# Kernel optimization log

Measured on AMD Instinct MI355X. Metric: run time of the kernel, lower is better.

Reference implementation:

```python
import jax, jax.numpy as jnp
import numpy as np

B, T, D, H = 2, 2048, 1024, 16
HD = D // H  # head dim = 64

def setup_inputs() -> dict:
    key = jax.random.key(0)
    k1, k2, k3 = jax.random.split(key, 3)
    x = jax.random.normal(k1, (B, T, D), dtype=jnp.float32)
    W_qkv = jax.random.normal(k2, (D, 3 * D), dtype=jnp.float32) * 0.02
    b_qkv = jax.random.normal(k3, (3 * D,), dtype=jnp.float32) * 0.02
    return {"x": x, "W_qkv": W_qkv, "b_qkv": b_qkv}

def reference(x, W_qkv, b_qkv):
    Bc, Tc, C = x.shape
    qkv = x @ W_qkv + b_qkv                     # [B,T,3D]
    q, k, v = jnp.split(qkv, 3, axis=-1)        # each [B,T,D]
    def to_heads(t):
        return t.reshape(Bc, Tc, H, HD).transpose(0, 2, 1, 3)  # [B,H,T,hd]
    q, k, v = to_heads(q), to_heads(k), to_heads(v)
    scale = 1.0 / jnp.sqrt(jnp.asarray(HD, dtype=x.dtype))
    att = jnp.einsum('bhqd,bhkd->bhqk', q, k) * scale  # [B,H,T,T]
    att = jax.nn.softmax(att, axis=-1)
    y = jnp.einsum('bhqk,bhkd->bhqd', att, v)          # [B,H,T,hd]
    return y.transpose(0, 2, 1, 3).reshape(Bc, Tc, C)
```

## Files before the change

### kernel.cpp

```cpp
#include <hip/hip_runtime.h>
#include <cstdint>

typedef unsigned short u16;
typedef __bf16 bf16x8 __attribute__((ext_vector_type(8)));
typedef float f32x4 __attribute__((ext_vector_type(4)));
typedef u16 u16x4 __attribute__((ext_vector_type(4)));
typedef u16 u16x8 __attribute__((ext_vector_type(8)));

static __device__ __forceinline__ u16 f2bf(float f) {
  return __builtin_bit_cast(u16, (__bf16)f);
}
static __device__ __forceinline__ float fexp2(float x) {
  float r;
  asm("v_exp_f32 %0, %1" : "=v"(r) : "v"(x));
  return r;
}

#define GLOAD16(gsrc, ldst) \
  __builtin_amdgcn_global_load_lds((const __attribute__((address_space(1))) void*)(gsrc), \
                                   (__attribute__((address_space(3))) void*)(ldst), 16, 0, 0)

#define WAIT_BAR_VM(n) do { \
    __builtin_amdgcn_sched_barrier(0); \
    asm volatile("s_waitcnt vmcnt(" #n ")" ::: "memory"); \
    __builtin_amdgcn_s_barrier(); \
    __builtin_amdgcn_sched_barrier(0); \
  } while (0)
#define WAIT_BAR_LGKM() do { \
    __builtin_amdgcn_sched_barrier(0); \
    asm volatile("s_waitcnt lgkmcnt(0)" ::: "memory"); \
    __builtin_amdgcn_s_barrier(); \
    __builtin_amdgcn_sched_barrier(0); \
  } while (0)

#define WV_VM(n) do { \
    __builtin_amdgcn_sched_barrier(0); \
    asm volatile("s_waitcnt vmcnt(" #n ")" ::: "memory"); \
    __builtin_amdgcn_sched_barrier(0); \
  } while (0)
#define WV_LGKM() do { \
    __builtin_amdgcn_sched_barrier(0); \
    asm volatile("s_waitcnt lgkmcnt(0)" ::: "memory"); \
    __builtin_amdgcn_sched_barrier(0); \
  } while (0)


__global__ __launch_bounds__(256) void k_prep(const float* __restrict__ x,
                                              const float* __restrict__ W,
                                              u16* __restrict__ xbf,
                                              u16* __restrict__ Wt) {
  __shared__ __align__(16) u16 tile[64 * 72];
  int t = threadIdx.x;
  if (blockIdx.x < 2048) {
    int idx = blockIdx.x * 256 + t;
    const float4* xv = (const float4*)x;
    float4 a = xv[(size_t)idx * 2];
    float4 b = xv[(size_t)idx * 2 + 1];
    u16x8 o;
    o[0]=f2bf(a.x); o[1]=f2bf(a.y); o[2]=f2bf(a.z); o[3]=f2bf(a.w);
    o[4]=f2bf(b.x); o[5]=f2bf(b.y); o[6]=f2bf(b.z); o[7]=f2bf(b.w);
    *(u16x8*)(xbf + (size_t)idx * 8) = o;
    return;
  }
  int bid = blockIdx.x - 2048;
  int bk = bid & 15, bn = bid >> 4;
  int k0 = bk * 64, n0 = bn * 64;
  #pragma unroll
  for (int r = 0; r < 4; r++) {
    int id = r * 256 + t;
    int kl = id >> 4;
    int c  = (id & 15) * 4;
    float4 v = *(const float4*)(W + (size_t)(k0 + kl) * 3072 + n0 + c);
    u16x4 o; o[0]=f2bf(v.x); o[1]=f2bf(v.y); o[2]=f2bf(v.z); o[3]=f2bf(v.w);
    *(u16x4*)(tile + kl * 72 + c) = o;
  }
  __syncthreads();
  #pragma unroll
  for (int r = 0; r < 2; r++) {
    int id = r * 256 + t;
    int nl = id >> 3;
    int w  = id & 7;
    u16x8 o;
    #pragma unroll
    for (int i = 0; i < 8; i++) o[i] = tile[(w * 8 + i) * 72 + nl];
    *(u16x8*)(Wt + (size_t)(n0 + nl) * 1024 + k0 + w * 8) = o;
  }
}

__global__ __launch_bounds__(256, 2) void k_gemm_qkv(const u16* __restrict__ xbf,
                                                     const u16* __restrict__ wt,
                                                     const float* __restrict__ bias,
                                                     u16* __restrict__ qkv,
                                                     u16* __restrict__ vT) {
  __shared__ __align__(16) u16 As[2 * 128 * 64];
  __shared__ __align__(16) u16 Bs[2 * 192 * 64];
  int wg = blockIdx.x;
  int swz = (wg & 7) * 64 + (wg >> 3);
  int mt = swz >> 4, nt = swz & 15;
  int m0 = mt * 128, n0 = nt * 192;
  int t = threadIdx.x;
  int lane = t & 63, wid = t >> 6;
  int wm = wid >> 1, wn = wid & 1;
  int g = lane >> 4, li = lane & 15;

  f32x4 acc[4][6];
  #pragma unroll
  for (int i = 0; i < 4; i++)
    #pragma unroll
    for (int j = 0; j < 6; j++) acc[i][j] = (f32x4){0.f, 0.f, 0.f, 0.f};

  auto stage = [&](int kt, int buf) {
    char* ad = (char*)As + buf * 16384;
    char* bd = (char*)Bs + buf * 24576;
    #pragma unroll
    for (int i = 0; i < 4; i++) {
      int p = t + i * 256;
      int row = p >> 3, ug = (p & 7) ^ (row & 7);
      GLOAD16(xbf + (size_t)(m0 + row) * 1024 + kt * 64 + ug * 8, ad + p * 16);
    }
    #pragma unroll
    for (int i = 0; i < 6; i++) {
      int p = t + i * 256;
      int row = p >> 3, ug = (p & 7) ^ (row & 7);
      GLOAD16(wt + (size_t)(n0 + row) * 1024 + kt * 64 + ug * 8, bd + p * 16);
    }
  };

  stage(0, 0);
  for (int kt = 0; kt < 16; ++kt) {
    if (kt < 15) {
      stage(kt + 1, (kt & 1) ^ 1);
      WAIT_BAR_VM(10);
    } else {
      WAIT_BAR_VM(0);
    }
    const char* ab = (const char*)As + (kt & 1) * 16384;
    const char* bb = (const char*)Bs + (kt & 1) * 24576;

    #pragma unroll
    for (int kk = 0; kk < 2; ++kk) {
      bf16x8 af[4], bfr[6];
      #pragma unroll
      for (int mi = 0; mi < 4; mi++) {
        int row = wm * 64 + mi * 16 + li;
        int u = (kk * 4 + g) ^ (row & 7);
        af[mi] = *(const bf16x8*)(ab + row * 128 + u * 16);
      }
      #pragma unroll
      for (int ni = 0; ni < 6; ni++) {
        int row = wn * 96 + ni * 16 + li;
        int u = (kk * 4 + g) ^ (row & 7);
        bfr[ni] = *(const bf16x8*)(bb + row * 128 + u * 16);
      }
      __builtin_amdgcn_s_setprio(1);
      #pragma unroll
      for (int mi = 0; mi < 4; mi++)
        #pragma unroll
        for (int ni = 0; ni < 6; ni++)
          acc[mi][ni] = __builtin_amdgcn_mfma_f32_16x16x32_bf16(af[mi], bfr[ni], acc[mi][ni], 0, 0, 0);
      __builtin_amdgcn_s_setprio(0);
    }

    WAIT_BAR_LGKM();
  }

  int b = m0 >> 11;
  int tbase = m0 & 2047;
  #pragma unroll
  for (int ni = 0; ni < 6; ni++) {
    int col = n0 + wn * 96 + ni * 16 + li;
    float bv = bias[col];
    float sc = (col < 1024) ? 0.18033688011112042f : 1.0f;
    #pragma unroll
    for (int mi = 0; mi < 4; mi++) {
      int trow = tbase + wm * 64 + mi * 16 + g * 4;
      if (col < 2048) {
        #pragma unroll
        for (int j = 0; j < 4; j++) {
          float v = (acc[mi][ni][j] + bv) * sc;
          qkv[(size_t)(b * 2048 + trow + j) * 3072 + col] = f2bf(v);
        }
      } else {
        u16x4 o;
        #pragma unroll
        for (int j = 0; j < 4; j++) o[j] = f2bf(acc[mi][ni][j] + bv);
        *(u16x4*)(vT + ((size_t)(b * 1024 + (col - 2048))) * 2048 + trow) = o;
      }
    }
  }
}

__global__ __launch_bounds__(128, 2) void k_attn(const u16* __restrict__ qkv,
                                                 const u16* __restrict__ vT,
                                                 float* __restrict__ out) {
  __shared__ __align__(16) u16 smem[16384];
  int bid = blockIdx.x;
  int bh = bid & 31, qt = bid >> 5;
  int b = bh >> 4, h = bh & 15;
  int qbase = qt * 64;
  int t = threadIdx.x, lane = t & 63, wave = t >> 6;
  int g = lane >> 4, li = lane & 15;

  bf16x8 q[4][2];
  #pragma unroll
  for (int qf = 0; qf < 4; qf++) {
    size_t qrow = (size_t)(b * 2048 + qbase + qf * 16 + li) * 3072 + h * 64;
    q[qf][0] = *(const bf16x8*)(qkv + qrow + g * 8);
    q[qf][1] = *(const bf16x8*)(qkv + qrow + 32 + g * 8);
  }

  f32x4 o[4][4];
  #pragma unroll
  for (int i = 0; i < 4; i++)
    #pragma unroll
    for (int j = 0; j < 4; j++) o[i][j] = (f32x4){0.f, 0.f, 0.f, 0.f};
  float la[4] = {0.f, 0.f, 0.f, 0.f};

  const u16* kbase_g = qkv + (size_t)(b * 2048 + wave * 1024) * 3072 + 1024 + h * 64;
  const u16* vbase_g = vT + (size_t)(bh * 64) * 2048 + wave * 1024;

  int r0 = lane >> 3, uu = lane & 7;
  int kuo = (uu ^ (r0 & 7)) * 8;
  int kR[8];
  #pragma unroll
  for (int i = 0; i < 8; i++) {
    int r = r0 + 8 * i;
    kR[i] = (r & 32) | ((r & 16) >> 2) | (((r >> 2) & 3) << 3) | (r & 3);
  }
  size_t vS0 = (size_t)r0 * 2048 + kuo;
  char* kd = (char*)smem + wave * 16384;
  char* vd = kd + 8192;

  auto stageK = [&](int key0) {
    #pragma unroll
    for (int i = 0; i < 8; i++)
      GLOAD16(kbase_g + (size_t)(key0 + kR[i]) * 3072 + kuo, kd + (lane + i * 64) * 16);
  };
  auto stageV = [&](int key0) {
    #pragma unroll
    for (int i = 0; i < 8; i++)
      GLOAD16(vbase_g + vS0 + (size_t)i * 16384 + key0, vd + (lane + i * 64) * 16);
  };

  stageK(0);
  stageV(0);
  WV_VM(0);

  int u0 = g ^ (li & 7);

  #pragma unroll 1
  for (int ph = 0; ph < 16; ++ph) {
    if (ph > 0) WV_VM(8);

    bf16x8 pb[4][2];
    #pragma unroll
    for (int b2 = 0; b2 < 2; ++b2) {
      f32x4 s[2][4];
      __builtin_amdgcn_s_setprio(1);
      #pragma unroll
      for (int st = 0; st < 2; ++st) {
        int row = (b2 * 2 + st) * 16 + li;
        bf16x8 kf0 = *(const bf16x8*)(kd + row * 128 + u0 * 16);
        bf16x8 kf1 = *(const bf16x8*)(kd + row * 128 + (u0 ^ 4) * 16);
        #pragma unroll
        for (int qf = 0; qf < 4; qf++) {
          f32x4 z = (f32x4){0.f, 0.f, 0.f, 0.f};
          s[st][qf] = __builtin_amdgcn_mfma_f32_16x16x32_bf16(kf0, q[qf][0], z, 0, 0, 0);
          s[st][qf] = __builtin_amdgcn_mfma_f32_16x16x32_bf16(kf1, q[qf][1], s[st][qf], 0, 0, 0);
        }
      }
      __builtin_amdgcn_s_setprio(0);
      #pragma unroll
      for (int qf = 0; qf < 4; qf++) {
        float p8[8];
        #pragma unroll
        for (int e = 0; e < 8; e++) p8[e] = fexp2(s[e >> 2][qf][e & 3]);
        la[qf] += ((p8[0] + p8[1]) + (p8[2] + p8[3])) + ((p8[4] + p8[5]) + (p8[6] + p8[7]));
        #pragma unroll
        for (int e = 0; e < 8; e++) pb[qf][b2][e] = (__bf16)p8[e];
      }
    }

    WV_LGKM();
    if (ph < 15) stageK((ph + 1) * 64);

    if (ph < 15) WV_VM(8); else WV_VM(0);

    __builtin_amdgcn_s_setprio(1);
    #pragma unroll
    for (int c = 0; c < 2; c++) {
      #pragma unroll
      for (int dt = 0; dt < 4; dt++) {
        int d = dt * 16 + li;
        bf16x8 vf = *(const bf16x8*)(vd + d * 128 + (((c * 4 + g) ^ (d & 7)) << 4));
        #pragma unroll
        for (int qf = 0; qf < 4; qf++)
          o[qf][dt] = __builtin_amdgcn_mfma_f32_16x16x32_bf16(vf, pb[qf][c], o[qf][dt], 0, 0, 0);
      }
    }
    __builtin_amdgcn_s_setprio(0);

    WV_LGKM();
    if (ph < 15) stageV((ph + 1) * 64);
  }

  #pragma unroll
  for (int qf = 0; qf < 4; qf++) {
    la[qf] += __shfl_xor(la[qf], 16);
    la[qf] += __shfl_xor(la[qf], 32);
  }

  float* pO = (float*)smem;
  float* pL = (float*)((char*)smem + 16384);
  __syncthreads();
  if (wave) {
    #pragma unroll
    for (int qf = 0; qf < 4; qf++) {
      int qq = qf * 16 + li;
      #pragma unroll
      for (int dt = 0; dt < 4; dt++) {
        int u = dt * 4 + g;
        *(f32x4*)((char*)pO + qq * 256 + ((u ^ (qq & 7)) << 4)) = o[qf][dt];
      }
      if (g == 0) pL[qq] = la[qf];
    }
  }
  __syncthreads();
  if (!wave) {
    #pragma unroll
    for (int qf = 0; qf < 4; qf++) {
      int qq = qf * 16 + li;
      float inv = 1.0f / (la[qf] + pL[qq]);
      size_t orow = (size_t)(b * 2048 + qbase + qq) * 1024 + h * 64;
      #pragma unroll
      for (int dt = 0; dt < 4; dt++) {
        int u = dt * 4 + g;
        f32x4 p2 = *(const f32x4*)((const char*)pO + qq * 256 + ((u ^ (qq & 7)) << 4));
        f32x4 r = (o[qf][dt] + p2) * inv;
        *(f32x4*)(out + orow + u * 4) = r;
      }
    }
  }
}

extern "C" void kernel_launch(void* const* d_in, const int* in_sizes, int n_in,
                              void* d_out, int out_size, void* d_ws, size_t ws_size,
                              hipStream_t stream) {
  const float* x    = (const float*)d_in[0];
  const float* W    = (const float*)d_in[1];
  const float* bias = (const float*)d_in[2];
  float* out = (float*)d_out;
  char* ws = (char*)d_ws;
  u16* xbf = (u16*)(ws + 0);
  u16* wt  = (u16*)(ws + 8388608);
  u16* qkv = (u16*)(ws + 14680064);
  u16* vt  = (u16*)(ws + 39845888);

  k_prep<<<2816, 256, 0, stream>>>(x, W, xbf, wt);
  k_gemm_qkv<<<512, 256, 0, stream>>>(xbf, wt, bias, qkv, vt);
  k_attn<<<1024, 128, 0, stream>>>(qkv, vt, out);
}
```

Baseline: 84.00 us.

## Split attention keys across four waves per block with smaller 32-key stages

The attention kernel now runs 256 threads (4 waves) per block instead of 2, so each wave handles 512 keys instead of 1024. Each wave stages 32 keys of K and V per phase (half the previous tile), which changes the LDS swizzles and the PV loop. The final reduction becomes a two-level tree across the four waves through LDS. The aim is more waves in flight and shorter per-wave serial loops, at the cost of more synchronisation in the combine step and smaller per-stage tiles.

```diff
diff --git a/kernel.cpp b/kernel.cpp
--- a/kernel.cpp
+++ b/kernel.cpp
@@ -190,10 +190,10 @@
   }
 }
 
-__global__ __launch_bounds__(128, 2) void k_attn(const u16* __restrict__ qkv,
+__global__ __launch_bounds__(256, 4) void k_attn(const u16* __restrict__ qkv,
                                                  const u16* __restrict__ vT,
                                                  float* __restrict__ out) {
-  __shared__ __align__(16) u16 smem[16384];
+  __shared__ __align__(16) u16 smem[16640];
   int bid = blockIdx.x;
   int bh = bid & 31, qt = bid >> 5;
   int b = bh >> 4, h = bh & 15;
@@ -216,30 +216,30 @@
     for (int j = 0; j < 4; j++) o[i][j] = (f32x4){0.f, 0.f, 0.f, 0.f};
   float la[4] = {0.f, 0.f, 0.f, 0.f};
 
-  const u16* kbase_g = qkv + (size_t)(b * 2048 + wave * 1024) * 3072 + 1024 + h * 64;
-  const u16* vbase_g = vT + (size_t)(bh * 64) * 2048 + wave * 1024;
-
-  int r0 = lane >> 3, uu = lane & 7;
-  int kuo = (uu ^ (r0 & 7)) * 8;
-  int kR[8];
-  #pragma unroll
-  for (int i = 0; i < 8; i++) {
-    int r = r0 + 8 * i;
-    kR[i] = (r & 32) | ((r & 16) >> 2) | (((r >> 2) & 3) << 3) | (r & 3);
-  }
-  size_t vS0 = (size_t)r0 * 2048 + kuo;
-  char* kd = (char*)smem + wave * 16384;
-  char* vd = kd + 8192;
+  const u16* kbase_g = qkv + (size_t)(b * 2048 + wave * 512) * 3072 + 1024 + h * 64;
+  const u16* vbase_g = vT + (size_t)(bh * 64) * 2048 + wave * 512;
+
+  int kCo = ((lane & 7) ^ (lane >> 3)) * 8;
+  int kR[4];
+  #pragma unroll
+  for (int i = 0; i < 4; i++) {
+    int r = (lane >> 3) + 8 * i;
+    kR[i] = ((r & 16) >> 2) | (((r >> 2) & 3) << 3) | (r & 3);
+  }
+  int vCo = ((lane & 3) ^ ((lane >> 3) & 3)) * 8;
+  char* kd = (char*)smem + wave * 8192;
+  char* vd = kd + 4096;
 
   auto stageK = [&](int key0) {
     #pragma unroll
-    for (int i = 0; i < 8; i++)
-      GLOAD16(kbase_g + (size_t)(key0 + kR[i]) * 3072 + kuo, kd + (lane + i * 64) * 16);
+    for (int i = 0; i < 4; i++)
+      GLOAD16(kbase_g + (size_t)(key0 + kR[i]) * 3072 + kCo, kd + (lane + i * 64) * 16);
   };
   auto stageV = [&](int key0) {
     #pragma unroll
-    for (int i = 0; i < 8; i++)
-      GLOAD16(vbase_g + vS0 + (size_t)i * 16384 + key0, vd + (lane + i * 64) * 16);
+    for (int i = 0; i < 4; i++)
+      GLOAD16(vbase_g + (size_t)((lane >> 2) + 16 * i) * 2048 + vCo + key0,
+              vd + (lane + i * 64) * 16);
   };
 
   stageK(0);
@@ -247,19 +247,19 @@
   WV_VM(0);
 
   int u0 = g ^ (li & 7);
+  int fv = (li >> 1) & 3;
 
   #pragma unroll 1
   for (int ph = 0; ph < 16; ++ph) {
-    if (ph > 0) WV_VM(8);
-
-    bf16x8 pb[4][2];
-    #pragma unroll
-    for (int b2 = 0; b2 < 2; ++b2) {
+    WV_VM(4);
+
+    bf16x8 pb[4];
+    {
       f32x4 s[2][4];
       __builtin_amdgcn_s_setprio(1);
       #pragma unroll
       for (int st = 0; st < 2; ++st) {
-        int row = (b2 * 2 + st) * 16 + li;
+        int row = st * 16 + li;
         bf16x8 kf0 = *(const bf16x8*)(kd + row * 128 + u0 * 16);
         bf16x8 kf1 = *(const bf16x8*)(kd + row * 128 + (u0 ^ 4) * 16);
         #pragma unroll
@@ -277,31 +277,31 @@
         for (int e = 0; e < 8; e++) p8[e] = fexp2(s[e >> 2][qf][e & 3]);
         la[qf] += ((p8[0] + p8[1]) + (p8[2] + p8[3])) + ((p8[4] + p8[5]) + (p8[6] + p8[7]));
         #pragma unroll
-        for (int e = 0; e < 8; e++) pb[qf][b2][e] = (__bf16)p8[e];
+        for (int e = 0; e < 8; e++) pb[qf][e] = (__bf16)p8[e];
       }
     }
 
     WV_LGKM();
-    if (ph < 15) stageK((ph + 1) * 64);
-
-    if (ph < 15) WV_VM(8); else WV_VM(0);
+    if (ph < 15) {
+      stageK((ph + 1) * 32);
+      WV_VM(4);
+    } else {
+      WV_VM(0);
+    }
 
     __builtin_amdgcn_s_setprio(1);
     #pragma unroll
-    for (int c = 0; c < 2; c++) {
-      #pragma unroll
-      for (int dt = 0; dt < 4; dt++) {
-        int d = dt * 16 + li;
-        bf16x8 vf = *(const bf16x8*)(vd + d * 128 + (((c * 4 + g) ^ (d & 7)) << 4));
-        #pragma unroll
-        for (int qf = 0; qf < 4; qf++)
-          o[qf][dt] = __builtin_amdgcn_mfma_f32_16x16x32_bf16(vf, pb[qf][c], o[qf][dt], 0, 0, 0);
-      }
+    for (int dt = 0; dt < 4; dt++) {
+      int d = dt * 16 + li;
+      bf16x8 vf = *(const bf16x8*)(vd + d * 64 + ((g ^ fv) << 4));
+      #pragma unroll
+      for (int qf = 0; qf < 4; qf++)
+        o[qf][dt] = __builtin_amdgcn_mfma_f32_16x16x32_bf16(vf, pb[qf], o[qf][dt], 0, 0, 0);
     }
     __builtin_amdgcn_s_setprio(0);
 
     WV_LGKM();
-    if (ph < 15) stageV((ph + 1) * 64);
+    if (ph < 15) stageV((ph + 1) * 32);
   }
 
   #pragma unroll
@@ -310,34 +310,60 @@
     la[qf] += __shfl_xor(la[qf], 32);
   }
 
-  float* pO = (float*)smem;
-  float* pL = (float*)((char*)smem + 16384);
-  __syncthreads();
-  if (wave) {
+  auto oAddr = [&](int a, int qq, int u) -> char* {
+    return (char*)smem + a * 16384 + qq * 256 + ((u ^ (qq & 7)) << 4);
+  };
+  float* laA0 = (float*)((char*)smem + 32768);
+  float* laA1 = (float*)((char*)smem + 33024);
+
+  __syncthreads();
+  if (wave >= 2) {
+    int a = wave - 2;
+    float* laA = a ? laA1 : laA0;
     #pragma unroll
     for (int qf = 0; qf < 4; qf++) {
       int qq = qf * 16 + li;
       #pragma unroll
-      for (int dt = 0; dt < 4; dt++) {
-        int u = dt * 4 + g;
-        *(f32x4*)((char*)pO + qq * 256 + ((u ^ (qq & 7)) << 4)) = o[qf][dt];
-      }
-      if (g == 0) pL[qq] = la[qf];
-    }
-  }
-  __syncthreads();
-  if (!wave) {
+      for (int dt = 0; dt < 4; dt++)
+        *(f32x4*)oAddr(a, qq, dt * 4 + g) = o[qf][dt];
+      if (g == 0) laA[qq] = la[qf];
+    }
+  }
+  __syncthreads();
+  if (wave < 2) {
+    float* laA = wave ? laA1 : laA0;
     #pragma unroll
     for (int qf = 0; qf < 4; qf++) {
       int qq = qf * 16 + li;
-      float inv = 1.0f / (la[qf] + pL[qq]);
+      #pragma unroll
+      for (int dt = 0; dt < 4; dt++)
+        o[qf][dt] += *(const f32x4*)oAddr(wave, qq, dt * 4 + g);
+      la[qf] += laA[qq];
+    }
+  }
+  __syncthreads();
+  if (wave == 1) {
+    #pragma unroll
+    for (int qf = 0; qf < 4; qf++) {
+      int qq = qf * 16 + li;
+      #pragma unroll
+      for (int dt = 0; dt < 4; dt++)
+        *(f32x4*)oAddr(0, qq, dt * 4 + g) = o[qf][dt];
+      if (g == 0) laA0[qq] = la[qf];
+    }
+  }
+  __syncthreads();
+  if (wave == 0) {
+    #pragma unroll
+    for (int qf = 0; qf < 4; qf++) {
+      int qq = qf * 16 + li;
+      float inv = 1.0f / (la[qf] + laA0[qq]);
       size_t orow = (size_t)(b * 2048 + qbase + qq) * 1024 + h * 64;
       #pragma unroll
       for (int dt = 0; dt < 4; dt++) {
-        int u = dt * 4 + g;
-        f32x4 p2 = *(const f32x4*)((const char*)pO + qq * 256 + ((u ^ (qq & 7)) << 4));
+        f32x4 p2 = *(const f32x4*)oAddr(0, qq, dt * 4 + g);
         f32x4 r = (o[qf][dt] + p2) * inv;
-        *(f32x4*)(out + orow + u * 4) = r;
+        *(f32x4*)(out + orow + (dt * 4 + g) * 4) = r;
       }
     }
   }
@@ -358,5 +384,5 @@
 
   k_prep<<<2816, 256, 0, stream>>>(x, W, xbf, wt);
   k_gemm_qkv<<<512, 256, 0, stream>>>(xbf, wt, bias, qkv, vt);
-  k_attn<<<1024, 128, 0, stream>>>(qkv, vt, out);
-}
+  k_attn<<<1024, 256, 0, stream>>>(qkv, vt, out);
+}
```

Measured after the change: 228.2 us. 2.72x slower.
